# Optimization experiments

Measured on AMD Instinct MI355X. Metric: run time of the kernel, lower is better.

The kernel has to match this reference:

```python
import jax, jax.numpy as jnp
import numpy as np

B, N, M = 256, 512, 512


def setup_inputs() -> dict:
    key = jax.random.key(0)
    kx, kw, kt = jax.random.split(key, 3)
    x = jax.random.uniform(kx, (B, N), dtype=jnp.float32)
    w = jax.random.uniform(kw, (N, M), dtype=jnp.float32)
    t = jax.random.uniform(kt, (B, M), dtype=jnp.float32)
    return {"x": x, "w": w, "t": t}


def reference(x, w, t):
    # x: [B, N], w: [N, M], t: [B, M]
    x3 = x[:, :, None]   # [B, N, 1]
    t3 = t[:, None, :]   # [B, 1, M]
    w3 = w[None, :, :]   # [1, N, M]

    # relevance of x per (n, m): sum over batch of min(x, t) / sum over batch of x
    rel_x = jnp.minimum(x3, t3).sum(axis=0, keepdims=True) / x3.sum(axis=0, keepdims=True)  # [1, N, M]
    # relevance of w per (b, m): sum over N of min(w, t) / sum over N of w
    rel_w = jnp.minimum(w3, t3).sum(axis=-2, keepdims=True) / w3.sum(axis=-2, keepdims=True)  # [B, 1, M]

    # argmax over the N (inner) dimension
    ind_w = jnp.argmax(jnp.minimum(x3, rel_x), axis=-2)  # [B, M]
    ind_x = jnp.argmax(jnp.minimum(rel_w, w3), axis=-2)  # [B, M]

    # inner_x and inner_w are numerically identical in forward (detach only affects grads)
    inner = jnp.minimum(x3, w3)  # [B, N, M]
    chosen_x = jnp.take_along_axis(inner, ind_x[:, None, :], axis=-2)[:, 0, :]  # [B, M]
    chosen_w = jnp.take_along_axis(inner, ind_w[:, None, :], axis=-2)[:, 0, :]  # [B, M]
    return (chosen_x, chosen_w)
```

## Files before the change

### kernel.cpp

```cpp
#include <hip/hip_runtime.h>

#define B 256
#define N 512
#define M 512
#define BM (B * M)
#define NM (N * M)

__device__ __forceinline__ void tile_tr256(const float* __restrict__ src,
                                           float* __restrict__ dst,
                                           int R, int C, int r0, int c0, int tid) {
    __shared__ float s[64][65];
    const int tx = tid & 63, q = tid >> 6;
    #pragma unroll
    for (int j = 0; j < 16; ++j) {
        int rl = q * 16 + j;
        s[rl][tx] = src[(r0 + rl) * C + c0 + tx];
    }
    __syncthreads();
    #pragma unroll
    for (int j = 0; j < 16; ++j) {
        int cl = q * 16 + j;
        dst[(c0 + cl) * R + r0 + tx] = s[tx][cl];
    }
}

__global__ __launch_bounds__(256) void k_a(const float* __restrict__ x,
                                           const float* __restrict__ w,
                                           const float* __restrict__ t,
                                           float* __restrict__ xT,
                                           float* __restrict__ wT,
                                           float* __restrict__ tT,
                                           float* __restrict__ sum_x,
                                           float* __restrict__ sum_w,
                                           float* __restrict__ px) {
    const int blk = blockIdx.x, tid = threadIdx.x;
    if (blk < 32) {
        tile_tr256(x, xT, B, N, (blk >> 3) * 64, (blk & 7) * 64, tid);
    } else if (blk < 96) {
        int id = blk - 32;
        tile_tr256(w, wT, N, M, (id >> 3) * 64, (id & 7) * 64, tid);
    } else if (blk < 128) {
        int id = blk - 96;
        tile_tr256(t, tT, B, M, (id >> 3) * 64, (id & 7) * 64, tid);
    } else if (blk < 130) {
        const int i = (blk - 128) * 256 + tid;
        double a0 = 0, a1 = 0, a2 = 0, a3 = 0;
        for (int b = 0; b < B; b += 4) {
            a0 += (double)x[(b + 0) * N + i];
            a1 += (double)x[(b + 1) * N + i];
            a2 += (double)x[(b + 2) * N + i];
            a3 += (double)x[(b + 3) * N + i];
        }
        sum_x[i] = (float)((a0 + a1) + (a2 + a3));
    } else if (blk < 132) {
        const int mm = (blk - 130) * 256 + tid;
        double a0 = 0, a1 = 0, a2 = 0, a3 = 0;
        for (int n = 0; n < N; n += 4) {
            a0 += (double)w[(n + 0) * M + mm];
            a1 += (double)w[(n + 1) * M + mm];
            a2 += (double)w[(n + 2) * M + mm];
            a3 += (double)w[(n + 3) * M + mm];
        }
        sum_w[mm] = (float)((a0 + a1) + (a2 + a3));
    } else {
        const int rb  = blk - 132;
        const int z   = rb >> 7;
        const int rem = rb & 127;
        const int m0 = (rem & 7) * 64;
        const int n0 = (rem >> 3) * 32;
        const int tx = tid & 15, ty = tid >> 4;
        __shared__ float s_t[32][64];
        __shared__ float s_x[32][36];
        const int sr = tid >> 3, sc = tid & 7;
        float aA0 = 0.f, aA1 = 0.f, aA2 = 0.f, aA3 = 0.f;
        float aB0 = 0.f, aB1 = 0.f, aB2 = 0.f, aB3 = 0.f;
        const int nA = ty * 2, nB = nA + 1;
        for (int scnk = 0; scnk < 2; ++scnk) {
            const int bb = z * 64 + scnk * 32;
            __syncthreads();
            *(float4*)&s_t[sr][sc * 8]     = *(const float4*)&t[(bb + sr) * M + m0 + sc * 8];
            *(float4*)&s_t[sr][sc * 8 + 4] = *(const float4*)&t[(bb + sr) * M + m0 + sc * 8 + 4];
            *(float4*)&s_x[sr][sc * 4]     = *(const float4*)&x[(bb + sr) * N + n0 + sc * 4];
            __syncthreads();
            #pragma unroll 8
            for (int i = 0; i < 32; ++i) {
                float4 tv = *(const float4*)&s_t[i][tx * 4];
                float xA = s_x[i][nA], xB = s_x[i][nB];
                aA0 += fminf(xA, tv.x); aA1 += fminf(xA, tv.y);
                aA2 += fminf(xA, tv.z); aA3 += fminf(xA, tv.w);
                aB0 += fminf(xB, tv.x); aB1 += fminf(xB, tv.y);
                aB2 += fminf(xB, tv.z); aB3 += fminf(xB, tv.w);
            }
        }
        __syncthreads();
        float* so = &s_t[0][0];
        so[(tx * 4 + 0) * 32 + nA] = aA0; so[(tx * 4 + 0) * 32 + nB] = aB0;
        so[(tx * 4 + 1) * 32 + nA] = aA1; so[(tx * 4 + 1) * 32 + nB] = aB1;
        so[(tx * 4 + 2) * 32 + nA] = aA2; so[(tx * 4 + 2) * 32 + nB] = aB2;
        so[(tx * 4 + 3) * 32 + nA] = aA3; so[(tx * 4 + 3) * 32 + nB] = aB3;
        __syncthreads();
        const int m_l = tid >> 2, n_l = (tid & 3) * 8;
        float* dst = &px[z * NM + (m0 + m_l) * N + n0 + n_l];
        *(float4*)&dst[0] = *(const float4*)&so[m_l * 32 + n_l];
        *(float4*)&dst[4] = *(const float4*)&so[m_l * 32 + n_l + 4];
    }
}

__global__ __launch_bounds__(512) void k_col(
        const float* __restrict__ x, const float* __restrict__ xT,
        const float* __restrict__ wT, const float* __restrict__ tT,
        const float* __restrict__ px, const float* __restrict__ sum_x,
        const float* __restrict__ sum_w, float* __restrict__ out) {
    const int m = blockIdx.x, tid = threadIdx.x;
    const int lane = tid & 63, wid = tid >> 6;

    __shared__ float  worig[512], pm[512], wsrt[512];
    __shared__ float  srx_r[512], srx_u[512];
    __shared__ int    srx_n[512];
    __shared__ int    cnt[256], cbase[256], cslot[256];
    __shared__ int    rcnt[256], rbase[256], rslot[256], rbmax[256];
    __shared__ double bsumI[256];
    __shared__ float  wtotmax[8], red3[3][8];
    __shared__ int    ctot[4], rtot[4];
    __shared__ double btot[4];

    const float wv = wT[m * N + tid];
    float p = px[m * N + tid];
    p += px[NM + m * N + tid];
    p += px[2 * NM + m * N + tid];
    p += px[3 * NM + m * N + tid];
    const float rv = p / sum_x[tid];
    worig[tid] = wv;
    if (tid < 256) { cnt[tid] = 0; rcnt[tid] = 0; cslot[tid] = 0; rslot[tid] = 0; rbmax[tid] = 0; }

    float pmv = wv;
    #pragma unroll
    for (int off = 1; off < 64; off <<= 1) {
        float o = __shfl_up(pmv, off, 64);
        if (lane >= off) pmv = fmaxf(pmv, o);
    }
    if (lane == 63) wtotmax[wid] = pmv;
    float wmn = wv, rmn = rv, rmx = rv;
    #pragma unroll
    for (int off = 32; off > 0; off >>= 1) {
        wmn = fminf(wmn, __shfl_xor(wmn, off, 64));
        rmn = fminf(rmn, __shfl_xor(rmn, off, 64));
        rmx = fmaxf(rmx, __shfl_xor(rmx, off, 64));
    }
    if (lane == 0) { red3[0][wid] = wmn; red3[1][wid] = rmn; red3[2][wid] = rmx; }
    __syncthreads();

    {
        float om = -1e30f;
        for (int j = 0; j < wid; ++j) om = fmaxf(om, wtotmax[j]);
        pm[tid] = fmaxf(pmv, om);
    }
    float wmin = red3[0][0], rmin = red3[1][0], rmax = red3[2][0], wmax = wtotmax[0];
    #pragma unroll
    for (int j = 1; j < 8; ++j) {
        wmin = fminf(wmin, red3[0][j]);
        rmin = fminf(rmin, red3[1][j]);
        rmax = fmaxf(rmax, red3[2][j]);
        wmax = fmaxf(wmax, wtotmax[j]);
    }

    const float wscale = 255.0f / fmaxf(wmax - wmin, 1e-30f);
    int wk = (int)((wv - wmin) * wscale);
    wk = wk < 0 ? 0 : (wk > 255 ? 255 : wk);
    atomicAdd(&cnt[wk], 1);
    const float rscale = 255.0f / fmaxf(rmax - rmin, 1e-30f);
    int rk;
    { int kv = (int)((rv - rmin) * rscale); kv = kv < 0 ? 0 : (kv > 255 ? 255 : kv); rk = 255 - kv; }
    atomicAdd(&rcnt[rk], 1);
    atomicMax(&rbmax[rk], __float_as_int(rv));
    __syncthreads();

    int myc = (tid < 256) ? cnt[tid] : rcnt[tid - 256];
    int incl = myc;
    #pragma unroll
    for (int off = 1; off < 64; off <<= 1) {
        int o = __shfl_up(incl, off, 64);
        if (lane >= off) incl += o;
    }
    if (lane == 63) { if (wid < 4) ctot[wid] = incl; else rtot[wid - 4] = incl; }
    __syncthreads();
    if (tid < 256) {
        int eo = 0;
        for (int j = 0; j < wid; ++j) eo += ctot[j];
        cbase[tid] = eo + incl - myc;
    } else {
        int eo = 0, w2 = wid - 4;
        for (int j = 0; j < w2; ++j) eo += rtot[j];
        rbase[tid - 256] = eo + incl - myc;
    }
    __syncthreads();

    { int p1 = cbase[wk] + atomicAdd(&cslot[wk], 1); wsrt[p1] = wv; }
    { int p2 = rbase[rk] + atomicAdd(&rslot[rk], 1);
      srx_r[p2] = rv; srx_n[p2] = tid; srx_u[p2] = __int_as_float(rbmax[rk]); }
    __syncthreads();

    double bincl = 0.0, mysum = 0.0;
    if (tid < 256) {
        int st = cbase[tid], e = st + cnt[tid];
        for (int i = st; i < e; ++i) mysum += (double)wsrt[i];
        bincl = mysum;
        #pragma unroll
        for (int off = 1; off < 64; off <<= 1) {
            double o = __shfl_up(bincl, off, 64);
            if (lane >= off) bincl += o;
        }
        if (lane == 63) btot[wid] = bincl;
    }
    __syncthreads();
    if (tid < 256) {
        double eo = 0.0;
        for (int j = 0; j < wid; ++j) eo += btot[j];
        bsumI[tid] = eo + bincl;
    }
    __syncthreads();

    if (tid < 256) {
        const int b = tid;
        float bv = -1.0f; int bi = 0;
        for (int i = 0; i < 512; ++i) {
            float u = srx_u[i];
            if (__ballot(u >= bv) == 0ULL) break;
            float r = srx_r[i];
            int   n = srx_n[i];
            float xv = xT[n * B + b];
            float v = fminf(xv, r);
            if (v > bv || (v == bv && n < bi)) { bv = v; bi = n; }
        }
        out[BM + b * M + m] = fminf(x[b * N + bi], worig[bi]);
    } else {
        const int b = tid - 256;
        const float tbm = tT[m * B + b];
        float btf = (tbm - wmin) * wscale;
        int kk; double S;
        if (btf < 0.0f) { kk = 0; S = 0.0; }
        else {
            int bt = (int)btf; bt = bt > 255 ? 255 : bt;
            kk = cbase[bt];
            S = (bt > 0) ? bsumI[bt - 1] : 0.0;
            int e = cbase[bt] + cnt[bt];
            for (int i = cbase[bt]; i < e; ++i) {
                float v = wsrt[i];
                if (v < tbm) { ++kk; S += (double)v; }
            }
        }
        double rw = S + (double)tbm * (double)(512 - kk);
        float c = (float)rw / sum_w[m];
        float tgt = fminf(c, pm[511]);
        int lo = 0, hi = 511;
        while (lo < hi) { int mid = (lo + hi) >> 1; if (pm[mid] >= tgt) hi = mid; else lo = mid + 1; }
        const int ind = lo;
        out[b * M + m] = fminf(x[b * N + ind], worig[ind]);
    }
}

extern "C" void kernel_launch(void* const* d_in, const int* in_sizes, int n_in,
                              void* d_out, int out_size, void* d_ws, size_t ws_size,
                              hipStream_t stream) {
    const float* x = (const float*)d_in[0];
    const float* w = (const float*)d_in[1];
    const float* t = (const float*)d_in[2];
    float* out = (float*)d_out;

    float* ws = (float*)d_ws;
    float* xT    = ws;
    float* wT    = ws + 131072;
    float* tT    = ws + 393216;
    float* sum_x = ws + 524288;
    float* sum_w = ws + 524800;
    float* px    = ws + 525312;

    k_a  <<<644, 256, 0, stream>>>(x, w, t, xT, wT, tT, sum_x, sum_w, px);
    k_col<<<512, 512, 0, stream>>>(x, xT, wT, tT, px, sum_x, sum_w, out);
}
```

Baseline: 90.05 us.

## Fuse prep and column kernels into one persistent kernel with grid barrier

Merges the two launches into a single 512-block kernel. The first phase does the transposes, sums and partial min-sums, with two 256-thread halves per block sharing a byte-addressed shared-memory pool. A flag-based global barrier follows, after which each block runs the per-column phase. The aim is to remove the second launch and the gap between kernels, at the cost of a memset launch, spin-waiting on flags, and reliance on all 512 blocks being co-resident (the spin has a timeout).

```diff
diff --git a/kernel.cpp b/kernel.cpp
--- a/kernel.cpp
+++ b/kernel.cpp
@@ -6,11 +6,16 @@
 #define BM (B * M)
 #define NM (N * M)
 
+
+#define HALF_BYTES 16640
+#define SMEM_BYTES 33280
+
 __device__ __forceinline__ void tile_tr256(const float* __restrict__ src,
                                            float* __restrict__ dst,
-                                           int R, int C, int r0, int c0, int tid) {
-    __shared__ float s[64][65];
-    const int tx = tid & 63, q = tid >> 6;
+                                           int R, int C, int r0, int c0,
+                                           int tl, char* hbase) {
+    float (*s)[65] = reinterpret_cast<float (*)[65]>(hbase);
+    const int tx = tl & 63, q = tl >> 6;
     #pragma unroll
     for (int j = 0; j < 16; ++j) {
         int rl = q * 16 + j;
@@ -24,26 +29,29 @@
     }
 }
 
-__global__ __launch_bounds__(256) void k_a(const float* __restrict__ x,
-                                           const float* __restrict__ w,
-                                           const float* __restrict__ t,
-                                           float* __restrict__ xT,
-                                           float* __restrict__ wT,
-                                           float* __restrict__ tT,
-                                           float* __restrict__ sum_x,
-                                           float* __restrict__ sum_w,
-                                           float* __restrict__ px) {
+__global__ __launch_bounds__(512, 4) void k_fused(
+        const float* __restrict__ x, const float* __restrict__ w,
+        const float* __restrict__ t,
+        float* __restrict__ xT, float* __restrict__ wT, float* __restrict__ tT,
+        float* __restrict__ sum_x, float* __restrict__ sum_w,
+        float* __restrict__ px, int* __restrict__ flags,
+        float* __restrict__ out) {
+    __shared__ __align__(16) char smem[SMEM_BYTES];
     const int blk = blockIdx.x, tid = threadIdx.x;
-    if (blk < 32) {
-        tile_tr256(x, xT, B, N, (blk >> 3) * 64, (blk & 7) * 64, tid);
-    } else if (blk < 96) {
-        int id = blk - 32;
-        tile_tr256(w, wT, N, M, (id >> 3) * 64, (id & 7) * 64, tid);
-    } else if (blk < 128) {
-        int id = blk - 96;
-        tile_tr256(t, tT, B, M, (id >> 3) * 64, (id & 7) * 64, tid);
-    } else if (blk < 130) {
-        const int i = (blk - 128) * 256 + tid;
+    const int half = tid >> 8, tl = tid & 255;
+    char* hbase = smem + half * HALF_BYTES;
+
+    if (blk < 16) {
+        const int u = blk * 2 + half;
+        tile_tr256(x, xT, B, N, (u >> 3) * 64, (u & 7) * 64, tl, hbase);
+    } else if (blk < 48) {
+        const int u = (blk - 16) * 2 + half;
+        tile_tr256(w, wT, N, M, (u >> 3) * 64, (u & 7) * 64, tl, hbase);
+    } else if (blk < 64) {
+        const int u = (blk - 48) * 2 + half;
+        tile_tr256(t, tT, B, M, (u >> 3) * 64, (u & 7) * 64, tl, hbase);
+    } else if (blk == 64) {
+        const int i = tid;
         double a0 = 0, a1 = 0, a2 = 0, a3 = 0;
         for (int b = 0; b < B; b += 4) {
             a0 += (double)x[(b + 0) * N + i];
@@ -52,8 +60,8 @@
             a3 += (double)x[(b + 3) * N + i];
         }
         sum_x[i] = (float)((a0 + a1) + (a2 + a3));
-    } else if (blk < 132) {
-        const int mm = (blk - 130) * 256 + tid;
+    } else if (blk == 65) {
+        const int mm = tid;
         double a0 = 0, a1 = 0, a2 = 0, a3 = 0;
         for (int n = 0; n < N; n += 4) {
             a0 += (double)w[(n + 0) * M + mm];
@@ -62,16 +70,16 @@
             a3 += (double)w[(n + 3) * M + mm];
         }
         sum_w[mm] = (float)((a0 + a1) + (a2 + a3));
-    } else {
-        const int rb  = blk - 132;
+    } else if (blk < 322) {
+        const int rb  = (blk - 66) * 2 + half;
         const int z   = rb >> 7;
         const int rem = rb & 127;
         const int m0 = (rem & 7) * 64;
         const int n0 = (rem >> 3) * 32;
-        const int tx = tid & 15, ty = tid >> 4;
-        __shared__ float s_t[32][64];
-        __shared__ float s_x[32][36];
-        const int sr = tid >> 3, sc = tid & 7;
+        const int tx = tl & 15, ty = tl >> 4;
+        float (*s_t)[64] = reinterpret_cast<float (*)[64]>(hbase);
+        float (*s_x)[36] = reinterpret_cast<float (*)[36]>(hbase + 8192);
+        const int sr = tl >> 3, sc = tl & 7;
         float aA0 = 0.f, aA1 = 0.f, aA2 = 0.f, aA3 = 0.f;
         float aB0 = 0.f, aB1 = 0.f, aB2 = 0.f, aB3 = 0.f;
         const int nA = ty * 2, nB = nA + 1;
@@ -99,30 +107,48 @@
         so[(tx * 4 + 2) * 32 + nA] = aA2; so[(tx * 4 + 2) * 32 + nB] = aB2;
         so[(tx * 4 + 3) * 32 + nA] = aA3; so[(tx * 4 + 3) * 32 + nB] = aB3;
         __syncthreads();
-        const int m_l = tid >> 2, n_l = (tid & 3) * 8;
+        const int m_l = tl >> 2, n_l = (tl & 3) * 8;
         float* dst = &px[z * NM + (m0 + m_l) * N + n0 + n_l];
         *(float4*)&dst[0] = *(const float4*)&so[m_l * 32 + n_l];
         *(float4*)&dst[4] = *(const float4*)&so[m_l * 32 + n_l + 4];
     }
-}
-
-__global__ __launch_bounds__(512) void k_col(
-        const float* __restrict__ x, const float* __restrict__ xT,
-        const float* __restrict__ wT, const float* __restrict__ tT,
-        const float* __restrict__ px, const float* __restrict__ sum_x,
-        const float* __restrict__ sum_w, float* __restrict__ out) {
-    const int m = blockIdx.x, tid = threadIdx.x;
+
+    __threadfence();
+    __syncthreads();
+    if (tid == 0) atomicExch(&flags[blk], 1);
+    {
+        int spins = 0;
+        while (__hip_atomic_load(&flags[tid], __ATOMIC_RELAXED,
+                                 __HIP_MEMORY_SCOPE_AGENT) == 0) {
+            __builtin_amdgcn_s_sleep(2);
+            if (++spins > (1 << 22)) break;
+        }
+    }
+    __threadfence();
+    __syncthreads();
+
+    const int m = blk;
     const int lane = tid & 63, wid = tid >> 6;
 
-    __shared__ float  worig[512], pm[512], wsrt[512];
-    __shared__ float  srx_r[512], srx_u[512];
-    __shared__ int    srx_n[512];
-    __shared__ int    cnt[256], cbase[256], cslot[256];
-    __shared__ int    rcnt[256], rbase[256], rslot[256], rbmax[256];
-    __shared__ double bsumI[256];
-    __shared__ float  wtotmax[8], red3[3][8];
-    __shared__ int    ctot[4], rtot[4];
-    __shared__ double btot[4];
+    double* bsumI   = (double*)(smem);
+    double* btot    = (double*)(smem + 2048);
+    float*  worig   = (float*)(smem + 2080);
+    float*  pm      = (float*)(smem + 4128);
+    float*  wsrt    = (float*)(smem + 6176);
+    float*  srx_r   = (float*)(smem + 8224);
+    float*  srx_u   = (float*)(smem + 10272);
+    int*    srx_n   = (int*)(smem + 12320);
+    int*    cnt     = (int*)(smem + 14368);
+    int*    cbase   = (int*)(smem + 15392);
+    int*    cslot   = (int*)(smem + 16416);
+    int*    rcnt    = (int*)(smem + 17440);
+    int*    rbase   = (int*)(smem + 18464);
+    int*    rslot   = (int*)(smem + 19488);
+    int*    rbmax   = (int*)(smem + 20512);
+    float*  wtotmax = (float*)(smem + 21536);
+    float (*red3)[8] = (float (*)[8])(smem + 21568);
+    int*    ctot    = (int*)(smem + 21664);
+    int*    rtot    = (int*)(smem + 21680);
 
     const float wv = wT[m * N + tid];
     float p = px[m * N + tid];
@@ -274,7 +300,9 @@
     float* sum_x = ws + 524288;
     float* sum_w = ws + 524800;
     float* px    = ws + 525312;
-
-    k_a  <<<644, 256, 0, stream>>>(x, w, t, xT, wT, tT, sum_x, sum_w, px);
-    k_col<<<512, 512, 0, stream>>>(x, xT, wT, tT, px, sum_x, sum_w, out);
+    int*   flags = (int*)(ws + 1573888);
+
+    hipMemsetAsync(flags, 0, 512 * sizeof(int), stream);
+    k_fused<<<512, 512, 0, stream>>>(x, w, t, xT, wT, tT,
+                                     sum_x, sum_w, px, flags, out);
 }
```

New measurement: 253.5 us. +181.5%, slower.

## Fold batch-split partials and column sums into single rel_x pass

Applied to the files above, without the earlier changes.

The min-sum kernel now loops over all four batch chunks inside one block, so each block writes the finished rel_x value (divided by the column sum of x, also computed in-block) instead of four partial planes. The separate sum_x and sum_w blocks are removed, and k_col computes the sum of w for its column from shared memory. This cuts global traffic for the partials and the reads of the four planes, and drops the grid from 644 to 256 blocks. In exchange, each compute block does four times the serial work with fewer blocks in flight, which lowers parallelism on this GPU.

```diff
diff --git a/kernel.cpp b/kernel.cpp
--- a/kernel.cpp
+++ b/kernel.cpp
@@ -4,7 +4,7 @@
 #define N 512
 #define M 512
 #define BM (B * M)
-#define NM (N * M)
+
 
 __device__ __forceinline__ void tile_tr256(const float* __restrict__ src,
                                            float* __restrict__ dst,
@@ -30,87 +30,82 @@
                                            float* __restrict__ xT,
                                            float* __restrict__ wT,
                                            float* __restrict__ tT,
-                                           float* __restrict__ sum_x,
-                                           float* __restrict__ sum_w,
-                                           float* __restrict__ px) {
+                                           float* __restrict__ rvp) {
     const int blk = blockIdx.x, tid = threadIdx.x;
-    if (blk < 32) {
-        tile_tr256(x, xT, B, N, (blk >> 3) * 64, (blk & 7) * 64, tid);
-    } else if (blk < 96) {
-        int id = blk - 32;
-        tile_tr256(w, wT, N, M, (id >> 3) * 64, (id & 7) * 64, tid);
-    } else if (blk < 128) {
-        int id = blk - 96;
-        tile_tr256(t, tT, B, M, (id >> 3) * 64, (id & 7) * 64, tid);
-    } else if (blk < 130) {
-        const int i = (blk - 128) * 256 + tid;
-        double a0 = 0, a1 = 0, a2 = 0, a3 = 0;
-        for (int b = 0; b < B; b += 4) {
-            a0 += (double)x[(b + 0) * N + i];
-            a1 += (double)x[(b + 1) * N + i];
-            a2 += (double)x[(b + 2) * N + i];
-            a3 += (double)x[(b + 3) * N + i];
-        }
-        sum_x[i] = (float)((a0 + a1) + (a2 + a3));
-    } else if (blk < 132) {
-        const int mm = (blk - 130) * 256 + tid;
-        double a0 = 0, a1 = 0, a2 = 0, a3 = 0;
-        for (int n = 0; n < N; n += 4) {
-            a0 += (double)w[(n + 0) * M + mm];
-            a1 += (double)w[(n + 1) * M + mm];
-            a2 += (double)w[(n + 2) * M + mm];
-            a3 += (double)w[(n + 3) * M + mm];
-        }
-        sum_w[mm] = (float)((a0 + a1) + (a2 + a3));
-    } else {
-        const int rb  = blk - 132;
-        const int z   = rb >> 7;
-        const int rem = rb & 127;
-        const int m0 = (rem & 7) * 64;
-        const int n0 = (rem >> 3) * 32;
+    if (blk < 128) {
+        const int m0 = (blk & 7) * 64;
+        const int n0 = (blk >> 3) * 32;
         const int tx = tid & 15, ty = tid >> 4;
-        __shared__ float s_t[32][64];
-        __shared__ float s_x[32][36];
+        __shared__ float  s_t[32][64];
+        __shared__ float  s_x[32][36];
+        __shared__ double sxc4[32][4];
         const int sr = tid >> 3, sc = tid & 7;
-        float aA0 = 0.f, aA1 = 0.f, aA2 = 0.f, aA3 = 0.f;
-        float aB0 = 0.f, aB1 = 0.f, aB2 = 0.f, aB3 = 0.f;
         const int nA = ty * 2, nB = nA + 1;
-        for (int scnk = 0; scnk < 2; ++scnk) {
-            const int bb = z * 64 + scnk * 32;
-            __syncthreads();
-            *(float4*)&s_t[sr][sc * 8]     = *(const float4*)&t[(bb + sr) * M + m0 + sc * 8];
-            *(float4*)&s_t[sr][sc * 8 + 4] = *(const float4*)&t[(bb + sr) * M + m0 + sc * 8 + 4];
-            *(float4*)&s_x[sr][sc * 4]     = *(const float4*)&x[(bb + sr) * N + n0 + sc * 4];
-            __syncthreads();
-            #pragma unroll 8
-            for (int i = 0; i < 32; ++i) {
-                float4 tv = *(const float4*)&s_t[i][tx * 4];
-                float xA = s_x[i][nA], xB = s_x[i][nB];
-                aA0 += fminf(xA, tv.x); aA1 += fminf(xA, tv.y);
-                aA2 += fminf(xA, tv.z); aA3 += fminf(xA, tv.w);
-                aB0 += fminf(xB, tv.x); aB1 += fminf(xB, tv.y);
-                aB2 += fminf(xB, tv.z); aB3 += fminf(xB, tv.w);
+        float pA0, pA1, pA2, pA3, pB0, pB1, pB2, pB3;
+        #pragma unroll
+        for (int z = 0; z < 4; ++z) {
+            float aA0 = 0.f, aA1 = 0.f, aA2 = 0.f, aA3 = 0.f;
+            float aB0 = 0.f, aB1 = 0.f, aB2 = 0.f, aB3 = 0.f;
+            for (int scnk = 0; scnk < 2; ++scnk) {
+                const int bb = z * 64 + scnk * 32;
+                __syncthreads();
+                *(float4*)&s_t[sr][sc * 8]     = *(const float4*)&t[(bb + sr) * M + m0 + sc * 8];
+                *(float4*)&s_t[sr][sc * 8 + 4] = *(const float4*)&t[(bb + sr) * M + m0 + sc * 8 + 4];
+                *(float4*)&s_x[sr][sc * 4]     = *(const float4*)&x[(bb + sr) * N + n0 + sc * 4];
+                __syncthreads();
+                #pragma unroll 8
+                for (int i = 0; i < 32; ++i) {
+                    float4 tv = *(const float4*)&s_t[i][tx * 4];
+                    float xA = s_x[i][nA], xB = s_x[i][nB];
+                    aA0 += fminf(xA, tv.x); aA1 += fminf(xA, tv.y);
+                    aA2 += fminf(xA, tv.z); aA3 += fminf(xA, tv.w);
+                    aB0 += fminf(xB, tv.x); aB1 += fminf(xB, tv.y);
+                    aB2 += fminf(xB, tv.z); aB3 += fminf(xB, tv.w);
+                }
             }
+            if (z == 0) {
+                pA0 = aA0; pA1 = aA1; pA2 = aA2; pA3 = aA3;
+                pB0 = aB0; pB1 = aB1; pB2 = aB2; pB3 = aB3;
+            } else {
+                pA0 += aA0; pA1 += aA1; pA2 += aA2; pA3 += aA3;
+                pB0 += aB0; pB1 += aB1; pB2 += aB2; pB3 += aB3;
+            }
+        }
+        if (tid < 128) {
+            const int col = n0 + (tid >> 2), ch = tid & 3;
+            double a = 0.0;
+            for (int b = ch; b < B; b += 4) a += (double)x[b * N + col];
+            sxc4[tid >> 2][ch] = a;
         }
         __syncthreads();
+        const float sA = (float)((sxc4[nA][0] + sxc4[nA][1]) + (sxc4[nA][2] + sxc4[nA][3]));
+        const float sB = (float)((sxc4[nB][0] + sxc4[nB][1]) + (sxc4[nB][2] + sxc4[nB][3]));
         float* so = &s_t[0][0];
-        so[(tx * 4 + 0) * 32 + nA] = aA0; so[(tx * 4 + 0) * 32 + nB] = aB0;
-        so[(tx * 4 + 1) * 32 + nA] = aA1; so[(tx * 4 + 1) * 32 + nB] = aB1;
-        so[(tx * 4 + 2) * 32 + nA] = aA2; so[(tx * 4 + 2) * 32 + nB] = aB2;
-        so[(tx * 4 + 3) * 32 + nA] = aA3; so[(tx * 4 + 3) * 32 + nB] = aB3;
+        so[(tx * 4 + 0) * 32 + nA] = pA0 / sA; so[(tx * 4 + 0) * 32 + nB] = pB0 / sB;
+        so[(tx * 4 + 1) * 32 + nA] = pA1 / sA; so[(tx * 4 + 1) * 32 + nB] = pB1 / sB;
+        so[(tx * 4 + 2) * 32 + nA] = pA2 / sA; so[(tx * 4 + 2) * 32 + nB] = pB2 / sB;
+        so[(tx * 4 + 3) * 32 + nA] = pA3 / sA; so[(tx * 4 + 3) * 32 + nB] = pB3 / sB;
         __syncthreads();
         const int m_l = tid >> 2, n_l = (tid & 3) * 8;
-        float* dst = &px[z * NM + (m0 + m_l) * N + n0 + n_l];
+        float* dst = &rvp[(m0 + m_l) * N + n0 + n_l];
         *(float4*)&dst[0] = *(const float4*)&so[m_l * 32 + n_l];
         *(float4*)&dst[4] = *(const float4*)&so[m_l * 32 + n_l + 4];
+    } else if (blk < 160) {
+        const int id = blk - 128;
+        tile_tr256(x, xT, B, N, (id >> 3) * 64, (id & 7) * 64, tid);
+    } else if (blk < 224) {
+        const int id = blk - 160;
+        tile_tr256(w, wT, N, M, (id >> 3) * 64, (id & 7) * 64, tid);
+    } else {
+        const int id = blk - 224;
+        tile_tr256(t, tT, B, M, (id >> 3) * 64, (id & 7) * 64, tid);
     }
 }
 
 __global__ __launch_bounds__(512) void k_col(
         const float* __restrict__ x, const float* __restrict__ xT,
         const float* __restrict__ wT, const float* __restrict__ tT,
-        const float* __restrict__ px, const float* __restrict__ sum_x,
-        const float* __restrict__ sum_w, float* __restrict__ out) {
+        const float* __restrict__ rvp, float* __restrict__ out) {
     const int m = blockIdx.x, tid = threadIdx.x;
     const int lane = tid & 63, wid = tid >> 6;
 
@@ -120,16 +115,13 @@
     __shared__ int    cnt[256], cbase[256], cslot[256];
     __shared__ int    rcnt[256], rbase[256], rslot[256], rbmax[256];
     __shared__ double bsumI[256];
+    __shared__ double swpart[4];
     __shared__ float  wtotmax[8], red3[3][8];
     __shared__ int    ctot[4], rtot[4];
     __shared__ double btot[4];
 
     const float wv = wT[m * N + tid];
-    float p = px[m * N + tid];
-    p += px[NM + m * N + tid];
-    p += px[2 * NM + m * N + tid];
-    p += px[3 * NM + m * N + tid];
-    const float rv = p / sum_x[tid];
+    const float rv = rvp[m * N + tid];
     worig[tid] = wv;
     if (tid < 256) { cnt[tid] = 0; rcnt[tid] = 0; cslot[tid] = 0; rslot[tid] = 0; rbmax[tid] = 0; }
 
@@ -149,6 +141,12 @@
     }
     if (lane == 0) { red3[0][wid] = wmn; red3[1][wid] = rmn; red3[2][wid] = rmx; }
     __syncthreads();
+
+    if (tid < 4) {
+        double a = 0.0;
+        for (int n = tid; n < 512; n += 4) a += (double)worig[n];
+        swpart[tid] = a;
+    }
 
     {
         float om = -1e30f;
@@ -250,7 +248,8 @@
             }
         }
         double rw = S + (double)tbm * (double)(512 - kk);
-        float c = (float)rw / sum_w[m];
+        const float sw = (float)((swpart[0] + swpart[1]) + (swpart[2] + swpart[3]));
+        float c = (float)rw / sw;
         float tgt = fminf(c, pm[511]);
         int lo = 0, hi = 511;
         while (lo < hi) { int mid = (lo + hi) >> 1; if (pm[mid] >= tgt) hi = mid; else lo = mid + 1; }
@@ -268,13 +267,11 @@
     float* out = (float*)d_out;
 
     float* ws = (float*)d_ws;
-    float* xT    = ws;
-    float* wT    = ws + 131072;
-    float* tT    = ws + 393216;
-    float* sum_x = ws + 524288;
-    float* sum_w = ws + 524800;
-    float* px    = ws + 525312;
-
-    k_a  <<<644, 256, 0, stream>>>(x, w, t, xT, wT, tT, sum_x, sum_w, px);
-    k_col<<<512, 512, 0, stream>>>(x, xT, wT, tT, px, sum_x, sum_w, out);
-}
+    float* xT  = ws;
+    float* wT  = ws + 131072;
+    float* tT  = ws + 393216;
+    float* rvp = ws + 524288;
+
+    k_a  <<<256, 256, 0, stream>>>(x, w, t, xT, wT, tT, rvp);
+    k_col<<<512, 512, 0, stream>>>(x, xT, wT, tT, rvp, out);
+}
```

After: 105.5 us. 1.17x slower.
